# Kernel tuning notes

Hardware: AMD Instinct MI355X
Metric: run time of the kernel (lower is better)

The kernel has to match this reference:

```python
import jax, jax.numpy as jnp
import numpy as np

N_NODES = 100000
N_EDGES = 1600000
D_IN, D_HID, D_OUT = 32, 16, 2


def graph_conv(x, edge_index, w_rel, w_root, b):
    # PyG GraphConv (aggr='add'): out_i = x_i @ W_root^T + (sum_{j in N(i)} x_j) @ W_rel^T + b
    src, dst = edge_index[0], edge_index[1]
    msgs = x[src]                                            # [E, d] neighbor gather
    agg = jax.ops.segment_sum(msgs, dst, num_segments=N_NODES)  # [N, d] scatter-add
    return agg @ w_rel.T + x @ w_root.T + b


def setup_inputs() -> dict:
    key = jax.random.key(0)
    ks = jax.random.split(key, 8)
    x = jax.random.normal(ks[0], (N_NODES, D_IN), dtype=jnp.float32)
    edge_index = jax.random.randint(ks[1], (2, N_EDGES), 0, N_NODES, dtype=jnp.int64)
    def glorot(k, shape):
        lim = np.sqrt(6.0 / (shape[0] + shape[1]))
        return jax.random.uniform(k, shape, jnp.float32, -lim, lim)
    w1_rel = glorot(ks[2], (D_HID, D_IN))
    w1_root = glorot(ks[3], (D_HID, D_IN))
    b1 = jnp.zeros((D_HID,), jnp.float32)
    w2_rel = glorot(ks[4], (D_OUT, D_HID))
    w2_root = glorot(ks[5], (D_OUT, D_HID))
    b2 = jnp.zeros((D_OUT,), jnp.float32)
    return {"x": x, "edge_index": edge_index,
            "w1_rel": w1_rel, "w1_root": w1_root, "b1": b1,
            "w2_rel": w2_rel, "w2_root": w2_root, "b2": b2}


def reference(x, edge_index, w1_rel, w1_root, b1, w2_rel, w2_root, b2):
    h = graph_conv(x, edge_index, w1_rel, w1_root, b1)
    h = jax.nn.relu(h)
    out = graph_conv(h, edge_index, w2_rel, w2_root, b2)
    return out
```

## Files before the change

kernel.cpp:

```cpp
#include <hip/hip_runtime.h>

#define N_NODES 100000
#define N_EDGES 1600000
#define D_IN 32
#define D_HID 16
#define D_OUT 2

#define NPB 128
#define NB 782
#define NROWS (NB * NPB)
#define CHUNK 4096
#define BBLOCKS ((N_EDGES + CHUNK - 1) / CHUNK)

#define PBC 2560
#define DUMMY_SRC 100000u
#define DUMMY_REC ((127u << 17) | DUMMY_SRC)
#define PAD_ALIGN 16

#define ACC2_K 16
#define ACC2_BPB 2
#define ACC2_BLOCKS (NB * ACC2_BPB)

__device__ __forceinline__ unsigned bfr(float x) {
    unsigned u = __float_as_uint(x);
    return (u + 0x7FFFu + ((u >> 16) & 1u)) >> 16;
}
__device__ __forceinline__ float bfu(unsigned lo16) {
    return __uint_as_float(lo16 << 16);
}

__global__ __launch_bounds__(512) void k_bin_node1(
    const int* __restrict__ ei, const float* __restrict__ x,
    const float* __restrict__ w_rel, const float* __restrict__ w_root,
    const float* __restrict__ bb,
    unsigned short* __restrict__ xr, float* __restrict__ agg,
    int* __restrict__ gcur, unsigned* __restrict__ recs2)
{
    __shared__ int cnt[NB];
    __shared__ int lcnt[NB];
    __shared__ int loff[NB];
    __shared__ int gbase[NB];
    __shared__ unsigned sorted[CHUNK];
    __shared__ unsigned short bkt16[CHUNK];
    __shared__ float s_rel[D_HID * D_IN];
    __shared__ float s_root[D_HID * D_IN];
    __shared__ float s_b[D_HID];
    int blk = blockIdx.x, tid = threadIdx.x;

    for (int i = tid; i < D_HID * D_IN; i += 512) {
        s_rel[i]  = w_rel[i];
        s_root[i] = w_root[i];
    }
    if (tid < D_HID) s_b[tid] = bb[tid];
    for (int i = tid; i < NB; i += 512) { cnt[i] = 0; lcnt[i] = 0; }
    __syncthreads();

    int e0 = blk * CHUNK;
    int e1 = min(e0 + CHUNK, N_EDGES);
    for (int e = e0 + tid; e < e1; e += 512)
        atomicAdd(&cnt[ei[N_EDGES + e] >> 7], 1);

    int node = blk * 512 + tid;
    if (node == N_NODES) {
        uint4* xp = (uint4*)(xr + (size_t)node * D_HID);
        xp[0] = make_uint4(0, 0, 0, 0);
        xp[1] = make_uint4(0, 0, 0, 0);
    } else if (node < N_NODES) {
        float row[D_IN];
        const float4* xp = (const float4*)(x + (size_t)node * D_IN);
#pragma unroll
        for (int i = 0; i < D_IN / 4; i++) {
            float4 v = xp[i];
            row[4*i+0] = v.x; row[4*i+1] = v.y; row[4*i+2] = v.z; row[4*i+3] = v.w;
        }
        float oa[D_HID], orr[D_HID];
#pragma unroll
        for (int o = 0; o < D_HID; o++) {
            float a = 0.f, r = s_b[o];
#pragma unroll
            for (int k = 0; k < D_IN; k++) {
                a += row[k] * s_rel[o * D_IN + k];
                r += row[k] * s_root[o * D_IN + k];
            }
            oa[o] = a; orr[o] = r;
        }
        unsigned p[8];
#pragma unroll
        for (int i = 0; i < 8; i++)
            p[i] = bfr(oa[2*i]) | (bfr(oa[2*i+1]) << 16);
        uint4* xrp = (uint4*)(xr + (size_t)node * D_HID);
        xrp[0] = make_uint4(p[0], p[1], p[2], p[3]);
        xrp[1] = make_uint4(p[4], p[5], p[6], p[7]);
        float4* aggp = (float4*)(agg + (size_t)node * D_HID);
#pragma unroll
        for (int i = 0; i < D_HID / 4; i++)
            aggp[i] = make_float4(orr[4*i], orr[4*i+1], orr[4*i+2], orr[4*i+3]);
    }
    __syncthreads();

    if (tid < 64) {
        int running = 0;
        for (int c = 0; c < (NB + 63) / 64; c++) {
            int idx = c * 64 + tid;
            int v = (idx < NB) ? cnt[idx] : 0;
            int incl = v;
#pragma unroll
            for (int off = 1; off < 64; off <<= 1) {
                int t = __shfl_up(incl, off);
                if (tid >= off) incl += t;
            }
            if (idx < NB) loff[idx] = running + incl - v;
            running += __shfl(incl, 63);
        }
    } else {
        for (int i = tid - 64; i < NB; i += 448)
            gbase[i] = (cnt[i] > 0) ? atomicAdd(&gcur[i], cnt[i]) : 0;
    }
    __syncthreads();

    for (int e = e0 + tid; e < e1; e += 512) {
        int src = ei[e];
        int dst = ei[N_EDGES + e];
        int bkt = dst >> 7;
        int r = atomicAdd(&lcnt[bkt], 1);
        int p = loff[bkt] + r;
        sorted[p] = ((unsigned)(dst & (NPB - 1)) << 17) | (unsigned)src;
        bkt16[p] = (unsigned short)bkt;
    }
    __syncthreads();

    int n4 = e1 - e0;
    for (int i = tid; i < n4; i += 512) {
        int b = bkt16[i];
        int idx = gbase[b] + (i - loff[b]);
        if (idx < PBC)
            recs2[b * PBC + idx] = sorted[i];
    }
}

__global__ __launch_bounds__(512) void k_sortacc(
    const int* __restrict__ gcur, unsigned* __restrict__ recs2,
    const unsigned short* __restrict__ srcf, float* __restrict__ dstf)
{
    __shared__ unsigned stage[PBC];
    __shared__ unsigned sorted[PBC];
    __shared__ int hist[NPB], sc[NPB], cur[NPB];
    int b = blockIdx.x, tid = threadIdx.x;
    int n = min(gcur[b], PBC);
    unsigned* w = recs2 + (size_t)b * PBC;

    if (tid < NPB) hist[tid] = 0;
    for (int i = tid; i < n; i += 512) stage[i] = w[i];
    __syncthreads();
    for (int i = tid; i < n; i += 512)
        atomicAdd(&hist[stage[i] >> 17], 1);
    __syncthreads();
    if (tid < NPB) sc[tid] = hist[tid];
    __syncthreads();
#pragma unroll
    for (int off = 1; off < NPB; off <<= 1) {
        int t = (tid >= off && tid < NPB) ? sc[tid - off] : 0;
        __syncthreads();
        if (tid < NPB) sc[tid] += t;
        __syncthreads();
    }
    if (tid < NPB) cur[tid] = sc[tid] - hist[tid];
    __syncthreads();
    for (int i = tid; i < n; i += 512) {
        unsigned r = stage[i];
        int slot = atomicAdd(&cur[r >> 17], 1);
        sorted[slot] = r;
    }
    int npad = (n + PAD_ALIGN - 1) & ~(PAD_ALIGN - 1);
    for (int i = n + tid; i < npad; i += 512) sorted[i] = DUMMY_REC;
    __syncthreads();

    for (int i = tid; i < npad; i += 512) w[i] = sorted[i];

    int g = tid >> 4;
    int f = tid & (D_HID - 1);
    int dbase = b * NPB;
    for (int base = g * 16; base < npad; base += 32 * 16) {
        unsigned e[16];
#pragma unroll
        for (int k = 0; k < 16; k++) e[k] = sorted[base + k];
        float v[16];
#pragma unroll
        for (int k = 0; k < 16; k++)
            v[k] = bfu(srcf[(e[k] & 0x1FFFF) * D_HID + f]);

        unsigned curd = e[0] >> 17;
        float acc = v[0];
#pragma unroll
        for (int k = 1; k < 16; k++) {
            unsigned dl = e[k] >> 17;
            if (dl == curd) {
                acc += v[k];
            } else {
                atomicAdd(&dstf[(dbase + curd) * D_HID + f], acc);
                curd = dl;
                acc = v[k];
            }
        }
        atomicAdd(&dstf[(dbase + curd) * D_HID + f], acc);
    }
}

__global__ __launch_bounds__(256) void k_node2h(
    const float* __restrict__ agg,
    const float* __restrict__ w_rel, const float* __restrict__ w_root,
    const float* __restrict__ b,
    float* __restrict__ hr, float* __restrict__ outv)
{
    __shared__ float s_rel[D_OUT * D_HID];
    __shared__ float s_root[D_OUT * D_HID];
    __shared__ float s_b[D_OUT];
    if (threadIdx.x < D_OUT * D_HID) {
        s_rel[threadIdx.x]  = w_rel[threadIdx.x];
        s_root[threadIdx.x] = w_root[threadIdx.x];
    }
    if (threadIdx.x < D_OUT) s_b[threadIdx.x] = b[threadIdx.x];
    __syncthreads();

    int node = blockIdx.x * blockDim.x + threadIdx.x;
    if (node > N_NODES) return;
    if (node == N_NODES) {
        ((float2*)hr)[node] = make_float2(0.f, 0.f);
        return;
    }

    float hv[D_HID];
    const float4* ap = (const float4*)(agg + (size_t)node * D_HID);
#pragma unroll
    for (int i = 0; i < D_HID / 4; i++) {
        float4 v = ap[i];
        hv[4*i+0] = fmaxf(v.x, 0.f); hv[4*i+1] = fmaxf(v.y, 0.f);
        hv[4*i+2] = fmaxf(v.z, 0.f); hv[4*i+3] = fmaxf(v.w, 0.f);
    }

    float o_rel[D_OUT], o_root[D_OUT];
#pragma unroll
    for (int o = 0; o < D_OUT; o++) {
        float a = 0.f, r = s_b[o];
#pragma unroll
        for (int k = 0; k < D_HID; k++) {
            a += hv[k] * s_rel[o * D_HID + k];
            r += hv[k] * s_root[o * D_HID + k];
        }
        o_rel[o] = a; o_root[o] = r;
    }
    ((float2*)hr)[node]   = make_float2(o_rel[0], o_rel[1]);
    ((float2*)outv)[node] = make_float2(o_root[0], o_root[1]);
}

__global__ __launch_bounds__(256) void k_acc2(
    const unsigned* __restrict__ recs2, const int* __restrict__ gcur,
    const float* __restrict__ hr, float* __restrict__ outv)
{
    int bucket = blockIdx.x / ACC2_BPB;
    int blk    = blockIdx.x % ACC2_BPB;
    int g = threadIdx.x >> 1;
    int f = threadIdx.x & 1;
    int r0 = (blk * 128 + g) * ACC2_K;
    int n = min(gcur[bucket], PBC);
    if (r0 >= n) return;
    const unsigned* rp = recs2 + (size_t)bucket * PBC + r0;

    unsigned e[ACC2_K];
#pragma unroll
    for (int k = 0; k < ACC2_K; k++) e[k] = rp[k];
    float v[ACC2_K];
#pragma unroll
    for (int k = 0; k < ACC2_K; k++)
        v[k] = hr[(e[k] & 0x1FFFF) * D_OUT + f];

    int dbase = bucket * NPB;
    unsigned cur = e[0] >> 17;
    float acc = v[0];
#pragma unroll
    for (int k = 1; k < ACC2_K; k++) {
        unsigned dl = e[k] >> 17;
        if (dl == cur) {
            acc += v[k];
        } else {
            int d = dbase + (int)cur;
            if (d < N_NODES) atomicAdd(&outv[d * D_OUT + f], acc);
            cur = dl;
            acc = v[k];
        }
    }
    int d = dbase + (int)cur;
    if (d < N_NODES) atomicAdd(&outv[d * D_OUT + f], acc);
}

extern "C" void kernel_launch(void* const* d_in, const int* in_sizes, int n_in,
                              void* d_out, int out_size, void* d_ws, size_t ws_size,
                              hipStream_t stream) {
    const float* x       = (const float*)d_in[0];
    const int*   ei      = (const int*)  d_in[1];
    const float* w1_rel  = (const float*)d_in[2];
    const float* w1_root = (const float*)d_in[3];
    const float* b1      = (const float*)d_in[4];
    const float* w2_rel  = (const float*)d_in[5];
    const float* w2_root = (const float*)d_in[6];
    const float* b2      = (const float*)d_in[7];
    float* out = (float*)d_out;

    float*          agg   = (float*)d_ws;
    unsigned short* xrh   = (unsigned short*)(agg + (size_t)NROWS * D_HID);
    unsigned*       recs2 = (unsigned*)(xrh + (size_t)NROWS * D_HID);
    float*          hr    = (float*)(recs2 + (size_t)NB * PBC);
    int*            gcur  = (int*)(hr + (size_t)NROWS * D_OUT);

    hipMemsetAsync(gcur, 0, NB * sizeof(int), stream);

    k_bin_node1<<<dim3(BBLOCKS), dim3(512), 0, stream>>>(
        ei, x, w1_rel, w1_root, b1, xrh, agg, gcur, recs2);

    k_sortacc<<<dim3(NB), dim3(512), 0, stream>>>(gcur, recs2, xrh, agg);

    k_node2h<<<dim3((N_NODES + 256) / 256), dim3(256), 0, stream>>>(
        agg, w2_rel, w2_root, b2, hr, out);

    k_acc2<<<dim3(ACC2_BLOCKS), dim3(256), 0, stream>>>(recs2, gcur, hr, out);
}
```

Before: 163.1 us.

## Fuse layer-2 node transform into sort-accumulate kernel with LDS aggregation tile

The layer-1 neighbor accumulation now goes into a padded shared-memory tile per bucket instead of global atomics. The same kernel then applies relu and the layer-2 root/rel projections for its 128 nodes, so the separate k_node2h launch and its global round-trip of the aggregate are gone. This swaps global float atomics for LDS atomics and removes one kernel launch. The cost is extra shared memory per block, which may lower occupancy.

```diff
diff --git a/kernel.cpp b/kernel.cpp
--- a/kernel.cpp
+++ b/kernel.cpp
@@ -33,7 +33,7 @@
     const int* __restrict__ ei, const float* __restrict__ x,
     const float* __restrict__ w_rel, const float* __restrict__ w_root,
     const float* __restrict__ bb,
-    unsigned short* __restrict__ xr, float* __restrict__ agg,
+    unsigned short* __restrict__ xr, float* __restrict__ aggr,
     int* __restrict__ gcur, unsigned* __restrict__ recs2)
 {
     __shared__ int cnt[NB];
@@ -91,7 +91,7 @@
         uint4* xrp = (uint4*)(xr + (size_t)node * D_HID);
         xrp[0] = make_uint4(p[0], p[1], p[2], p[3]);
         xrp[1] = make_uint4(p[4], p[5], p[6], p[7]);
-        float4* aggp = (float4*)(agg + (size_t)node * D_HID);
+        float4* aggp = (float4*)(aggr + (size_t)node * D_HID);
 #pragma unroll
         for (int i = 0; i < D_HID / 4; i++)
             aggp[i] = make_float4(orr[4*i], orr[4*i+1], orr[4*i+2], orr[4*i+3]);
@@ -140,16 +140,29 @@
 
 __global__ __launch_bounds__(512) void k_sortacc(
     const int* __restrict__ gcur, unsigned* __restrict__ recs2,
-    const unsigned short* __restrict__ srcf, float* __restrict__ dstf)
+    const unsigned short* __restrict__ srcf, const float* __restrict__ aggr,
+    const float* __restrict__ w2rel, const float* __restrict__ w2root,
+    const float* __restrict__ b2,
+    float* __restrict__ hr, float* __restrict__ outv)
 {
     __shared__ unsigned stage[PBC];
     __shared__ unsigned sorted[PBC];
+    __shared__ float tile[NPB * 17];
     __shared__ int hist[NPB], sc[NPB], cur[NPB];
+    __shared__ float s_rel[D_OUT * D_HID];
+    __shared__ float s_root[D_OUT * D_HID];
+    __shared__ float s_b2[D_OUT];
     int b = blockIdx.x, tid = threadIdx.x;
     int n = min(gcur[b], PBC);
     unsigned* w = recs2 + (size_t)b * PBC;
 
     if (tid < NPB) hist[tid] = 0;
+    if (tid < D_OUT * D_HID) {
+        s_rel[tid]  = w2rel[tid];
+        s_root[tid] = w2root[tid];
+    }
+    if (tid < D_OUT) s_b2[tid] = b2[tid];
+    for (int i = tid; i < NPB * 17; i += 512) tile[i] = 0.f;
     for (int i = tid; i < n; i += 512) stage[i] = w[i];
     __syncthreads();
     for (int i = tid; i < n; i += 512)
@@ -179,7 +192,6 @@
 
     int g = tid >> 4;
     int f = tid & (D_HID - 1);
-    int dbase = b * NPB;
     for (int base = g * 16; base < npad; base += 32 * 16) {
         unsigned e[16];
 #pragma unroll
@@ -197,60 +209,47 @@
             if (dl == curd) {
                 acc += v[k];
             } else {
-                atomicAdd(&dstf[(dbase + curd) * D_HID + f], acc);
+                atomicAdd(&tile[curd * 17 + f], acc);
                 curd = dl;
                 acc = v[k];
             }
         }
-        atomicAdd(&dstf[(dbase + curd) * D_HID + f], acc);
-    }
-}
-
-__global__ __launch_bounds__(256) void k_node2h(
-    const float* __restrict__ agg,
-    const float* __restrict__ w_rel, const float* __restrict__ w_root,
-    const float* __restrict__ b,
-    float* __restrict__ hr, float* __restrict__ outv)
-{
-    __shared__ float s_rel[D_OUT * D_HID];
-    __shared__ float s_root[D_OUT * D_HID];
-    __shared__ float s_b[D_OUT];
-    if (threadIdx.x < D_OUT * D_HID) {
-        s_rel[threadIdx.x]  = w_rel[threadIdx.x];
-        s_root[threadIdx.x] = w_root[threadIdx.x];
-    }
-    if (threadIdx.x < D_OUT) s_b[threadIdx.x] = b[threadIdx.x];
-    __syncthreads();
-
-    int node = blockIdx.x * blockDim.x + threadIdx.x;
-    if (node > N_NODES) return;
-    if (node == N_NODES) {
-        ((float2*)hr)[node] = make_float2(0.f, 0.f);
-        return;
-    }
-
-    float hv[D_HID];
-    const float4* ap = (const float4*)(agg + (size_t)node * D_HID);
-#pragma unroll
-    for (int i = 0; i < D_HID / 4; i++) {
-        float4 v = ap[i];
-        hv[4*i+0] = fmaxf(v.x, 0.f); hv[4*i+1] = fmaxf(v.y, 0.f);
-        hv[4*i+2] = fmaxf(v.z, 0.f); hv[4*i+3] = fmaxf(v.w, 0.f);
-    }
-
-    float o_rel[D_OUT], o_root[D_OUT];
-#pragma unroll
-    for (int o = 0; o < D_OUT; o++) {
-        float a = 0.f, r = s_b[o];
-#pragma unroll
-        for (int k = 0; k < D_HID; k++) {
-            a += hv[k] * s_rel[o * D_HID + k];
-            r += hv[k] * s_root[o * D_HID + k];
-        }
-        o_rel[o] = a; o_root[o] = r;
-    }
-    ((float2*)hr)[node]   = make_float2(o_rel[0], o_rel[1]);
-    ((float2*)outv)[node] = make_float2(o_root[0], o_root[1]);
+        atomicAdd(&tile[curd * 17 + f], acc);
+    }
+    __syncthreads();
+
+    if (tid < NPB) {
+        int node = b * NPB + tid;
+        if (node < N_NODES) {
+            float hv[D_HID];
+            const float4* ap = (const float4*)(aggr + (size_t)node * D_HID);
+#pragma unroll
+            for (int i = 0; i < D_HID / 4; i++) {
+                float4 r = ap[i];
+                hv[4*i+0] = fmaxf(r.x + tile[tid * 17 + 4*i+0], 0.f);
+                hv[4*i+1] = fmaxf(r.y + tile[tid * 17 + 4*i+1], 0.f);
+                hv[4*i+2] = fmaxf(r.z + tile[tid * 17 + 4*i+2], 0.f);
+                hv[4*i+3] = fmaxf(r.w + tile[tid * 17 + 4*i+3], 0.f);
+            }
+            float o_rel[D_OUT], o_root[D_OUT];
+#pragma unroll
+            for (int o = 0; o < D_OUT; o++) {
+                float a = 0.f, r = s_b2[o];
+#pragma unroll
+                for (int k = 0; k < D_HID; k++) {
+                    a += hv[k] * s_rel[o * D_HID + k];
+                    r += hv[k] * s_root[o * D_HID + k];
+                }
+                o_rel[o] = a; o_root[o] = r;
+            }
+            ((float2*)hr)[node]   = make_float2(o_rel[0], o_rel[1]);
+            ((float2*)outv)[node] = make_float2(o_root[0], o_root[1]);
+        }
+    }
+    if (b == NB - 1 && tid >= NPB && tid < NPB + 8) {
+        int node = N_NODES + (tid - NPB);
+        if (node < NROWS) ((float2*)hr)[node] = make_float2(0.f, 0.f);
+    }
 }
 
 __global__ __launch_bounds__(256) void k_acc2(
@@ -306,8 +305,8 @@
     const float* b2      = (const float*)d_in[7];
     float* out = (float*)d_out;
 
-    float*          agg   = (float*)d_ws;
-    unsigned short* xrh   = (unsigned short*)(agg + (size_t)NROWS * D_HID);
+    float*          aggr  = (float*)d_ws;
+    unsigned short* xrh   = (unsigned short*)(aggr + (size_t)NROWS * D_HID);
     unsigned*       recs2 = (unsigned*)(xrh + (size_t)NROWS * D_HID);
     float*          hr    = (float*)(recs2 + (size_t)NB * PBC);
     int*            gcur  = (int*)(hr + (size_t)NROWS * D_OUT);
@@ -315,12 +314,10 @@
     hipMemsetAsync(gcur, 0, NB * sizeof(int), stream);
 
     k_bin_node1<<<dim3(BBLOCKS), dim3(512), 0, stream>>>(
-        ei, x, w1_rel, w1_root, b1, xrh, agg, gcur, recs2);
-
-    k_sortacc<<<dim3(NB), dim3(512), 0, stream>>>(gcur, recs2, xrh, agg);
-
-    k_node2h<<<dim3((N_NODES + 256) / 256), dim3(256), 0, stream>>>(
-        agg, w2_rel, w2_root, b2, hr, out);
+        ei, x, w1_rel, w1_root, b1, xrh, aggr, gcur, recs2);
+
+    k_sortacc<<<dim3(NB), dim3(512), 0, stream>>>(
+        gcur, recs2, xrh, aggr, w2_rel, w2_root, b2, hr, out);
 
     k_acc2<<<dim3(ACC2_BLOCKS), dim3(256), 0, stream>>>(recs2, gcur, hr, out);
 }
```

After: 164.1 us. Within noise of the previous version (+0.6%).
